# Optimization experiments

Hardware: AMD Instinct MI355X
Metric: run time of the kernel (lower is better)

## Reference

```python
import jax, jax.numpy as jnp
import numpy as np

# Detector / Siddon constants (from init_kwargs)
H, W = 200, 200
DELX, DELY = 1.5, 1.5
NXV, NYV, NZV = 256, 256, 256  # voxel counts
EPS = 1e-8


def setup_inputs() -> dict:
    key = jax.random.key(0)
    kvol, = jax.random.split(key, 1)
    volume = jax.random.uniform(kvol, (NXV, NYV, NZV), dtype=jnp.float32)  # CT intensities
    spacing = jnp.ones((3,), jnp.float32)                                  # 1mm isotropic
    sdr = jnp.array([300.0], jnp.float32)                                  # source-to-detector radius
    rotations = jnp.array([[0.5, -0.2, 0.3]], jnp.float32)                 # theta, phi, gamma
    translations = jnp.array([[128.0, 128.0, 128.0]], jnp.float32)         # volume center (bx,by,bz)
    return {"volume": volume, "spacing": spacing, "sdr": sdr,
            "rotations": rotations, "translations": translations}


def _rotation_matrix(rotations):
    # R = Rz(theta) @ Ry(phi) @ Rx(gamma), batched
    theta, phi, gamma = rotations[:, 0], rotations[:, 1], rotations[:, 2]
    ct, st = jnp.cos(theta), jnp.sin(theta)
    cp, sp = jnp.cos(phi), jnp.sin(phi)
    cg, sg = jnp.cos(gamma), jnp.sin(gamma)
    z = jnp.zeros_like(theta)
    o = jnp.ones_like(theta)
    Rz = jnp.stack([ct, -st, z, st, ct, z, z, z, o], -1).reshape(-1, 3, 3)
    Ry = jnp.stack([cp, z, sp, z, o, z, -sp, z, cp], -1).reshape(-1, 3, 3)
    Rx = jnp.stack([o, z, z, z, cg, -sg, z, sg, cg], -1).reshape(-1, 3, 3)
    return Rz @ Ry @ Rx


def _make_xrays(sdr, rotations, translations):
    # Detector.make_xrays: source on column 0 of sdr*R, detector center opposite,
    # detector plane spanned by unit columns 1 and 2.
    R = _rotation_matrix(rotations)                 # (b,3,3), orthonormal columns
    source = sdr[:, None] * R[..., 0]               # (b,3)
    center = -source
    basis = jnp.stack([R[..., 1], R[..., 2]], 1)    # (b,2,3)
    source = source + translations
    center = center + translations
    t = (jnp.arange(-(H // 2), H // 2, dtype=jnp.float32) + 1.0) * DELX
    s = (jnp.arange(-(W // 2), W // 2, dtype=jnp.float32) + 1.0) * DELY
    coefs = jnp.stack(jnp.meshgrid(t, s, indexing="ij"), -1).reshape(-1, 2)  # (H*W,2) == cartesian_prod(t,s)
    target = jnp.einsum("bcd,nc->bnd", basis, coefs) + center[:, None, :]    # (b,n,3)
    return source[:, None, :], target               # (b,1,3), (b,n,3)


def reference(volume, spacing, sdr, rotations, translations):
    source, target = _make_xrays(sdr, rotations, translations)
    vol = jnp.flip(volume, 0)                       # Siddon flips axis 0
    nx, ny, nz = vol.shape
    sdd = target - source + EPS                     # (b,n,3) ray directions

    # Alphas at every axis-aligned plane intersection: P = (nx+1)+(ny+1)+(nz+1)
    alphas = jnp.concatenate(
        [(jnp.arange(n + 1, dtype=jnp.float32) * spacing[i] - source[..., i:i + 1]) / sdd[..., i:i + 1]
         for i, n in enumerate((nx, ny, nz))], axis=-1)          # (b,n,P)

    # Entry/exit alphas of the volume bounding box
    extent = jnp.asarray([nx, ny, nz], jnp.float32) * spacing
    a0 = (0.0 - source) / sdd
    a1 = (extent - source) / sdd
    amin = jnp.max(jnp.minimum(a0, a1), -1, keepdims=True)       # (b,n,1)
    amax = jnp.min(jnp.maximum(a0, a1), -1, keepdims=True)

    # Out-of-range alphas -> sentinel amax (sorts to the end, contributes zero step;
    # equivalent to the original's NaN + nansum handling)
    valid = (alphas >= amin) & (alphas <= amax)
    alphas = jnp.sort(jnp.where(valid, alphas, amax), axis=-1)

    mid = 0.5 * (alphas[..., :-1] + alphas[..., 1:])             # (b,n,P-1)
    step = jnp.diff(alphas, axis=-1)

    # Midpoint positions -> voxel indices (trunc, clamped in-bounds)
    xyz = source[:, :, None, :] + mid[..., None] * sdd[:, :, None, :]  # (b,n,P-1,3)
    idx = jnp.trunc(xyz / spacing).astype(jnp.int32)
    ix = jnp.clip(idx[..., 0], 0, nx - 1)
    iy = jnp.clip(idx[..., 1], 0, ny - 1)
    iz = jnp.clip(idx[..., 2], 0, nz - 1)
    voxels = vol[ix, iy, iz]                                     # gather, (b,n,P-1)

    drr = jnp.sum(voxels * step, -1) * jnp.linalg.norm(sdd, axis=-1)
    return drr.reshape(-1, H, W)
```

## Files before the change

kernel.cpp:

```cpp
#include <hip/hip_runtime.h>

#define H_ 200
#define W_ 200
#define DELX_ 1.5f
#define DELY_ 1.5f
#define NXV_ 256
#define NYV_ 256
#define NZV_ 256
#define EPS_ 1e-8f
#define NSEG 8
#define PPB 32
#define TILE_R 8
#define TILE_C 4
#define TILES_PER_IMG ((H_ / TILE_R) * (W_ / TILE_C))

__device__ __forceinline__ float alpha_mul(float k, float sp, float src, float inv_sdd) {
    return (k * sp - src) * inv_sdd;
}

__global__ void __launch_bounds__(256)
drr_fused(const float* __restrict__ vol,
          const float* __restrict__ spacing,
          const float* __restrict__ sdr,
          const float* __restrict__ rot,
          const float* __restrict__ trans,
          float* __restrict__ out) {
    const int t = threadIdx.x;
    const int pixLocal = t & (PPB - 1);
    const int seg = t >> 5;

    const int b   = blockIdx.x / TILES_PER_IMG;
    const int rem = blockIdx.x % TILES_PER_IMG;
    const int ty  = rem / (W_ / TILE_C);
    const int tx  = rem % (W_ / TILE_C);
    const int i = ty * TILE_R + (pixLocal >> 2);
    const int j = tx * TILE_C + (pixLocal & 3);
    const int pix = b * (H_ * W_) + i * W_ + j;

    const float theta = rot[b * 3 + 0], phi = rot[b * 3 + 1], gamma = rot[b * 3 + 2];
    const float ct = cosf(theta), st = sinf(theta);
    const float cp = cosf(phi),   sp = sinf(phi);
    const float cg = cosf(gamma), sg = sinf(gamma);
    const float r00 = ct * cp,                r10 = st * cp,                r20 = -sp;
    const float r01 = ct * sp * sg - st * cg, r11 = st * sp * sg + ct * cg, r21 = cp * sg;
    const float r02 = ct * sp * cg + st * sg, r12 = st * sp * cg - ct * sg, r22 = cp * cg;

    const float sd = sdr[b];
    const float tx_ = trans[b * 3 + 0], ty_ = trans[b * 3 + 1], tz_ = trans[b * 3 + 2];
    const float sx = sd * r00 + tx_, sy = sd * r10 + ty_, sz = sd * r20 + tz_;
    const float cxx = -sd * r00 + tx_, cyy = -sd * r10 + ty_, czz = -sd * r20 + tz_;

    const float tco = ((float)(i - H_ / 2) + 1.0f) * DELX_;
    const float sco = ((float)(j - W_ / 2) + 1.0f) * DELY_;
    const float gx = r01 * tco + r02 * sco + cxx;
    const float gy = r11 * tco + r12 * sco + cyy;
    const float gz = r21 * tco + r22 * sco + czz;

    const float dx = gx - sx + EPS_;
    const float dy = gy - sy + EPS_;
    const float dz = gz - sz + EPS_;

    const float spx = spacing[0], spy = spacing[1], spz = spacing[2];
    const float inv_spx = 1.0f / spx, inv_spy = 1.0f / spy, inv_spz = 1.0f / spz;
    const float inv_dx = 1.0f / dx, inv_dy = 1.0f / dy, inv_dz = 1.0f / dz;

    const float a0x = alpha_mul(0.f, spx, sx, inv_dx), a1x = alpha_mul((float)NXV_, spx, sx, inv_dx);
    const float a0y = alpha_mul(0.f, spy, sy, inv_dy), a1y = alpha_mul((float)NYV_, spy, sy, inv_dy);
    const float a0z = alpha_mul(0.f, spz, sz, inv_dz), a1z = alpha_mul((float)NZV_, spz, sz, inv_dz);

    const float amin = fmaxf(fmaxf(fminf(a0x, a1x), fminf(a0y, a1y)), fminf(a0z, a1z));
    const float amax = fminf(fminf(fmaxf(a0x, a1x), fmaxf(a0y, a1y)), fmaxf(a0z, a1z));

    const float norm = sqrtf(dx * dx + dy * dy + dz * dz);

    const float klo = (float)(seg * (NXV_ / NSEG));
    const float khi = (float)((seg + 1) * (NXV_ / NSEG));
    const float aA = alpha_mul(klo, spx, sx, inv_dx);
    const float aB = alpha_mul(khi, spx, sx, inv_dx);
    const float lo = fminf(aA, aB), hi = fmaxf(aA, aB);

    const float start = fmaxf(amin, lo);
    const float end   = fminf(amax, hi);

    float acc = 0.0f;
    if (start < end) {
        float kx, ky, kz, axv, ayv, azv, dkx, dky, dkz;
        {
            float kf = (start * dx + sx) * inv_spx;
            if (dx > 0.f) { dkx = 1.f;  kx = floorf(kf) + 1.f; }
            else          { dkx = -1.f; kx = ceilf(kf) - 1.f; }
            axv = alpha_mul(kx, spx, sx, inv_dx);
        }
        {
            float kf = (start * dy + sy) * inv_spy;
            if (dy > 0.f) { dky = 1.f;  ky = floorf(kf) + 1.f; }
            else          { dky = -1.f; ky = ceilf(kf) - 1.f; }
            ayv = alpha_mul(ky, spy, sy, inv_dy);
        }
        {
            float kf = (start * dz + sz) * inv_spz;
            if (dz > 0.f) { dkz = 1.f;  kz = floorf(kf) + 1.f; }
            else          { dkz = -1.f; kz = ceilf(kf) - 1.f; }
            azv = alpha_mul(kz, spz, sz, inv_dz);
        }

        float a_cur = start;
        for (int g = 0; g < 40; ++g) {
            float stp[4];
            int   off[4];
            float an_last;
            #pragma unroll
            for (int u = 0; u < 4; ++u) {
                float an = fminf(axv, fminf(ayv, azv));
                bool ok = (an <= end);
                stp[u] = ok ? (an - a_cur) : 0.0f;
                float midv = 0.5f * (a_cur + an);
                float x = (sx + midv * dx) * inv_spx;
                float y = (sy + midv * dy) * inv_spy;
                float z = (sz + midv * dz) * inv_spz;
                int ix = (int)x;
                int iy = (int)y;
                int iz = (int)z;
                ix = min(max(ix, 0), NXV_ - 1);
                iy = min(max(iy, 0), NYV_ - 1);
                iz = min(max(iz, 0), NZV_ - 1);
                off[u] = ((NXV_ - 1 - ix) * NYV_ + iy) * NZV_ + iz;
                a_cur = an;
                bool cx = (axv == an), cy = (ayv == an), cz = (azv == an);
                kx = cx ? kx + dkx : kx;
                ky = cy ? ky + dky : ky;
                kz = cz ? kz + dkz : kz;
                axv = alpha_mul(kx, spx, sx, inv_dx);
                ayv = alpha_mul(ky, spy, sy, inv_dy);
                azv = alpha_mul(kz, spz, sz, inv_dz);
                an_last = an;
            }
            float v0 = vol[off[0]];
            float v1 = vol[off[1]];
            float v2 = vol[off[2]];
            float v3 = vol[off[3]];
            acc += v0 * stp[0];
            acc += v1 * stp[1];
            acc += v2 * stp[2];
            acc += v3 * stp[3];
            if (an_last > end) break;
        }
    }
    float result = acc * norm;

    __shared__ float red[NSEG * PPB];
    red[t] = result;
    __syncthreads();
    if (t < PPB) {
        const int ii = ty * TILE_R + (t >> 2);
        const int jj = tx * TILE_C + (t & 3);
        const int opix = b * (H_ * W_) + ii * W_ + jj;
        float s = 0.0f;
        #pragma unroll
        for (int k = 0; k < NSEG; k++) s += red[t + k * PPB];
        out[opix] = s;
    }
}

extern "C" void kernel_launch(void* const* d_in, const int* in_sizes, int n_in,
                              void* d_out, int out_size, void* d_ws, size_t ws_size,
                              hipStream_t stream) {
    const float* vol     = (const float*)d_in[0];
    const float* spacing = (const float*)d_in[1];
    const float* sdr     = (const float*)d_in[2];
    const float* rot     = (const float*)d_in[3];
    const float* trans   = (const float*)d_in[4];
    float* out = (float*)d_out;

    const int B = in_sizes[2];
    const int nblocks = B * TILES_PER_IMG;
    drr_fused<<<nblocks, NSEG * PPB, 0, stream>>>(vol, spacing, sdr, rot, trans, out);
}
```

Measured before the change: 126.1 us.

## Software-pipeline Siddon ray marching with double-buffered voxel gathers

The march now takes 8 steps per group instead of 4 and alternates between two buffers. The voxel loads for one group are issued, then the next group's offsets and step lengths are computed while those loads are in flight, and only then are the loaded values accumulated. The goal is to hide global-memory gather latency behind the address arithmetic. The cost is more registers per thread, one wasted march computed past the end, and a lower step cap (7 double iterations, 112 steps plus the initial group) that could cut off long segments.

```diff
diff --git a/kernel.cpp b/kernel.cpp
--- a/kernel.cpp
+++ b/kernel.cpp
@@ -13,6 +13,8 @@
 #define TILE_R 8
 #define TILE_C 4
 #define TILES_PER_IMG ((H_ / TILE_R) * (W_ / TILE_C))
+#define G_ 8
+#define MAXGG 7
 
 __device__ __forceinline__ float alpha_mul(float k, float sp, float src, float inv_sdd) {
     return (k * sp - src) * inv_sdd;
@@ -35,7 +37,6 @@
     const int tx  = rem % (W_ / TILE_C);
     const int i = ty * TILE_R + (pixLocal >> 2);
     const int j = tx * TILE_C + (pixLocal & 3);
-    const int pix = b * (H_ * W_) + i * W_ + j;
 
     const float theta = rot[b * 3 + 0], phi = rot[b * 3 + 1], gamma = rot[b * 3 + 2];
     const float ct = cosf(theta), st = sinf(theta);
@@ -105,12 +106,11 @@
         }
 
         float a_cur = start;
-        for (int g = 0; g < 40; ++g) {
-            float stp[4];
-            int   off[4];
-            float an_last;
+
+        auto march8 = [&](float* stp, int* off) -> float {
+            float an_l = a_cur;
             #pragma unroll
-            for (int u = 0; u < 4; ++u) {
+            for (int u = 0; u < G_; ++u) {
                 float an = fminf(axv, fminf(ayv, azv));
                 bool ok = (an <= end);
                 stp[u] = ok ? (an - a_cur) : 0.0f;
@@ -133,17 +133,34 @@
                 axv = alpha_mul(kx, spx, sx, inv_dx);
                 ayv = alpha_mul(ky, spy, sy, inv_dy);
                 azv = alpha_mul(kz, spz, sz, inv_dz);
-                an_last = an;
+                an_l = an;
             }
-            float v0 = vol[off[0]];
-            float v1 = vol[off[1]];
-            float v2 = vol[off[2]];
-            float v3 = vol[off[3]];
-            acc += v0 * stp[0];
-            acc += v1 * stp[1];
-            acc += v2 * stp[2];
-            acc += v3 * stp[3];
-            if (an_last > end) break;
+            return an_l;
+        };
+
+        float stpA[G_], stpB[G_];
+        int   offA[G_], offB[G_];
+        float vA[G_], vB[G_];
+
+        float anA = march8(stpA, offA);
+        float anB;
+
+        for (int gg = 0; gg < MAXGG; ++gg) {
+            #pragma unroll
+            for (int u = 0; u < G_; ++u) vA[u] = vol[offA[u]];
+            bool doneA = anA > end;
+            anB = march8(stpB, offB);
+            #pragma unroll
+            for (int u = 0; u < G_; ++u) acc += vA[u] * stpA[u];
+            if (doneA) break;
+
+            #pragma unroll
+            for (int u = 0; u < G_; ++u) vB[u] = vol[offB[u]];
+            bool doneB = anB > end;
+            anA = march8(stpA, offA);
+            #pragma unroll
+            for (int u = 0; u < G_; ++u) acc += vB[u] * stpB[u];
+            if (doneB) break;
         }
     }
     float result = acc * norm;
```

New measurement: 133.6 us. 5.9% more time.

## Split rays into 16 x-segments across two blocks with a combine pass

Applied to the files above, without the earlier changes.

Each ray is now split into 16 segments along x instead of 8, spread over two blocks per 8x8 pixel tile. Each block writes per-half partial sums to workspace, and a second kernel adds the two halves. The inner traversal is unrolled to 8 steps per group with 8 gathers issued together, and the group count is capped at 10. The aim is more parallelism and more loads in flight per ray. The cost is an extra kernel launch and workspace traffic, and the MAXG*G_=80 step cap per segment must still cover every crossing in a 16-voxel slab.

```diff
diff --git a/kernel.cpp b/kernel.cpp
--- a/kernel.cpp
+++ b/kernel.cpp
@@ -8,34 +8,38 @@
 #define NYV_ 256
 #define NZV_ 256
 #define EPS_ 1e-8f
-#define NSEG 8
-#define PPB 32
+#define NSEG 16
+#define SEGS_PER_BLK 8
 #define TILE_R 8
-#define TILE_C 4
+#define TILE_C 8
 #define TILES_PER_IMG ((H_ / TILE_R) * (W_ / TILE_C))
+#define G_ 8
+#define MAXG 10
 
 __device__ __forceinline__ float alpha_mul(float k, float sp, float src, float inv_sdd) {
     return (k * sp - src) * inv_sdd;
 }
 
-__global__ void __launch_bounds__(256)
-drr_fused(const float* __restrict__ vol,
-          const float* __restrict__ spacing,
-          const float* __restrict__ sdr,
-          const float* __restrict__ rot,
-          const float* __restrict__ trans,
-          float* __restrict__ out) {
+__global__ void __launch_bounds__(512, 8)
+drr_partial(const float* __restrict__ vol,
+            const float* __restrict__ spacing,
+            const float* __restrict__ sdr,
+            const float* __restrict__ rot,
+            const float* __restrict__ trans,
+            float* __restrict__ partials,
+            int npix) {
     const int t = threadIdx.x;
-    const int pixLocal = t & (PPB - 1);
-    const int seg = t >> 5;
+    const int pixLocal = t & 63;
+    const int half = blockIdx.x & 1;
+    const int seg = (t >> 6) + (half << 3);
+    const int tileBlk = blockIdx.x >> 1;
 
-    const int b   = blockIdx.x / TILES_PER_IMG;
-    const int rem = blockIdx.x % TILES_PER_IMG;
-    const int ty  = rem / (W_ / TILE_C);
-    const int tx  = rem % (W_ / TILE_C);
-    const int i = ty * TILE_R + (pixLocal >> 2);
-    const int j = tx * TILE_C + (pixLocal & 3);
-    const int pix = b * (H_ * W_) + i * W_ + j;
+    const int b    = tileBlk / TILES_PER_IMG;
+    const int rem  = tileBlk % TILES_PER_IMG;
+    const int ty   = rem / (W_ / TILE_C);
+    const int tx   = rem % (W_ / TILE_C);
+    const int i = ty * TILE_R + (pixLocal >> 3);
+    const int j = tx * TILE_C + (pixLocal & 7);
 
     const float theta = rot[b * 3 + 0], phi = rot[b * 3 + 1], gamma = rot[b * 3 + 2];
     const float ct = cosf(theta), st = sinf(theta);
@@ -105,12 +109,12 @@
         }
 
         float a_cur = start;
-        for (int g = 0; g < 40; ++g) {
-            float stp[4];
-            int   off[4];
+        for (int g = 0; g < MAXG; ++g) {
+            float stp[G_];
+            int   off[G_];
             float an_last;
             #pragma unroll
-            for (int u = 0; u < 4; ++u) {
+            for (int u = 0; u < G_; ++u) {
                 float an = fminf(axv, fminf(ayv, azv));
                 bool ok = (an <= end);
                 stp[u] = ok ? (an - a_cur) : 0.0f;
@@ -135,31 +139,35 @@
                 azv = alpha_mul(kz, spz, sz, inv_dz);
                 an_last = an;
             }
-            float v0 = vol[off[0]];
-            float v1 = vol[off[1]];
-            float v2 = vol[off[2]];
-            float v3 = vol[off[3]];
-            acc += v0 * stp[0];
-            acc += v1 * stp[1];
-            acc += v2 * stp[2];
-            acc += v3 * stp[3];
+            float v[G_];
+            #pragma unroll
+            for (int u = 0; u < G_; ++u) v[u] = vol[off[u]];
+            #pragma unroll
+            for (int u = 0; u < G_; ++u) acc += v[u] * stp[u];
             if (an_last > end) break;
         }
     }
     float result = acc * norm;
 
-    __shared__ float red[NSEG * PPB];
+    __shared__ float red[SEGS_PER_BLK * 64];
     red[t] = result;
     __syncthreads();
-    if (t < PPB) {
-        const int ii = ty * TILE_R + (t >> 2);
-        const int jj = tx * TILE_C + (t & 3);
+    if (t < 64) {
+        const int ii = ty * TILE_R + (t >> 3);
+        const int jj = tx * TILE_C + (t & 7);
         const int opix = b * (H_ * W_) + ii * W_ + jj;
         float s = 0.0f;
         #pragma unroll
-        for (int k = 0; k < NSEG; k++) s += red[t + k * PPB];
-        out[opix] = s;
+        for (int k = 0; k < SEGS_PER_BLK; k++) s += red[t + k * 64];
+        partials[(size_t)half * npix + opix] = s;
     }
+}
+
+__global__ void __launch_bounds__(256)
+drr_combine(const float* __restrict__ partials, float* __restrict__ out, int npix) {
+    int pix = blockIdx.x * blockDim.x + threadIdx.x;
+    if (pix >= npix) return;
+    out[pix] = partials[pix] + partials[(size_t)npix + pix];
 }
 
 extern "C" void kernel_launch(void* const* d_in, const int* in_sizes, int n_in,
@@ -173,6 +181,10 @@
     float* out = (float*)d_out;
 
     const int B = in_sizes[2];
-    const int nblocks = B * TILES_PER_IMG;
-    drr_fused<<<nblocks, NSEG * PPB, 0, stream>>>(vol, spacing, sdr, rot, trans, out);
+    const int npix = B * H_ * W_;
+    float* partials = (float*)d_ws;
+
+    const int nblocks = B * TILES_PER_IMG * 2;
+    drr_partial<<<nblocks, 64 * SEGS_PER_BLK, 0, stream>>>(vol, spacing, sdr, rot, trans, partials, npix);
+    drr_combine<<<(npix + 255) / 256, 256, 0, stream>>>(partials, out, npix);
 }
```

Measured after the change: 120.6 us. 4.3% less time.
